# Performance work log

Hardware: AMD Instinct MI355X
Metric: run time of the kernel (lower is better)

The kernel has to match this reference:

```python
import jax, jax.numpy as jnp
import numpy as np

D, H, E, C, B = 1024, 2048, 8, 1024, 8192


def setup_inputs() -> dict:
    key = jax.random.key(0)
    ks = jax.random.split(key, 12)
    s_d = 1.0 / np.sqrt(D)
    s_h = 1.0 / np.sqrt(H)
    return {
        "x": jax.random.normal(ks[0], (B, D), dtype=jnp.float32),
        # gate (Router): Linear(D,D) -> relu -> Linear(D,E) -> softmax
        "gate_w1": jax.random.normal(ks[1], (D, D), dtype=jnp.float32) * s_d,
        "gate_b1": jax.random.normal(ks[2], (D,), dtype=jnp.float32) * s_d,
        "gate_w2": jax.random.normal(ks[3], (D, E), dtype=jnp.float32) * s_d,
        "gate_b2": jax.random.normal(ks[4], (E,), dtype=jnp.float32) * s_d,
        # experts stacked: fc1 [E,D,H], fc2 [E,H,H]
        "W1": jax.random.normal(ks[5], (E, D, H), dtype=jnp.float32) * s_d,
        "b1": jax.random.normal(ks[6], (E, H), dtype=jnp.float32) * s_d,
        "W2": jax.random.normal(ks[7], (E, H, H), dtype=jnp.float32) * s_h,
        "b2": jax.random.normal(ks[8], (E, H), dtype=jnp.float32) * s_h,
        # classifier Linear(H, C)
        "clf_w": jax.random.normal(ks[9], (H, C), dtype=jnp.float32) * s_h,
        "clf_b": jax.random.normal(ks[10], (C,), dtype=jnp.float32) * s_h,
    }


def reference(x, gate_w1, gate_b1, gate_w2, gate_b2, W1, b1, W2, b2, clf_w, clf_b):
    # Router: softmax over experts (dim=1)
    g = jax.nn.relu(x @ gate_w1 + gate_b1)          # [B, D]
    scores = jax.nn.softmax(g @ gate_w2 + gate_b2, axis=1)  # [B, E]

    # All experts, dense (training-mode forward): batched GEMMs over E
    h = jax.nn.relu(jnp.einsum('bd,edh->beh', x, W1) + b1[None])   # [B, E, H]
    expert_outs = jnp.einsum('beh,ehk->bek', h, W2) + b2[None]      # [B, E, H]

    # Shared classifier applied per (token, expert)
    logits = jnp.einsum('beh,hc->bec', expert_outs, clf_w) + clf_b  # [B, E, C]
    return logits, scores
```

## Files before the change

### kernel.cpp

```cpp
#include <hip/hip_runtime.h>
#include <stdint.h>

#define B_DIM 8192
#define D_DIM 1024
#define H_DIM 2048
#define E_DIM 8
#define C_DIM 1024

typedef _Float16 f16x8 __attribute__((ext_vector_type(8)));
typedef float f32x4 __attribute__((ext_vector_type(4)));

__device__ __forceinline__ void store_val(float* p, float v) { *p = v; }
__device__ __forceinline__ void store_val(_Float16* p, float v) { *p = (_Float16)v; }

__device__ __forceinline__ void async_cp16(const void* g, void* l) {
  __builtin_amdgcn_global_load_lds((const __attribute__((address_space(1))) void*)g,
                                   (__attribute__((address_space(3))) void*)l, 16, 0, 0);
}

template <bool RELU, bool BIAS, typename OUT_T>
__global__ void __launch_bounds__(256) gemm_bt(
    const _Float16* __restrict__ A, long aZ,
    const _Float16* __restrict__ Bt, long bZ,
    const float* __restrict__ bias, long biasZ,
    OUT_T* __restrict__ out, long outZ,
    int K, long rs)
{
  __shared__ _Float16 ldsA[128 * 64];
  __shared__ _Float16 ldsB[128 * 64];

  const int z = blockIdx.z;
  A   += (size_t)z * aZ;
  Bt  += (size_t)z * bZ;
  if (BIAS) bias += (size_t)z * biasZ;
  out += (size_t)z * outZ;

  const int tid  = threadIdx.x;
  const int wave = tid >> 6;
  const int lane = tid & 63;
  const int q    = lane >> 4;
  const int l16  = lane & 15;
  const int l8   = lane >> 3;
  const int l7   = lane & 7;

  const int m0   = blockIdx.y * 128;
  const int n0   = blockIdx.x * 128;
  const int wrow = (wave >> 1) * 64;
  const int wcol = (wave & 1) * 64;

  const int swz_st = ((l7 ^ l8) << 3);
  const _Float16* pa[4];
  const _Float16* pb[4];
#pragma unroll
  for (int i = 0; i < 4; ++i) {
    int ci = wave * 4 + i;
    pa[i] = A  + (size_t)(m0 + ci * 8 + l8) * K + swz_st;
    pb[i] = Bt + (size_t)(n0 + ci * 8 + l8) * K + swz_st;
  }

  int a_off[2][4], b_off[2][4];
#pragma unroll
  for (int kk = 0; kk < 2; ++kk) {
#pragma unroll
    for (int r = 0; r < 4; ++r) {
      int sw = ((kk * 4 + q) ^ (l16 & 7)) << 4;
      a_off[kk][r] = (wrow + r * 16 + l16) * 128 + sw;
      b_off[kk][r] = (wcol + r * 16 + l16) * 128 + sw;
    }
  }

  f32x4 acc[4][4];
#pragma unroll
  for (int r = 0; r < 4; ++r)
#pragma unroll
    for (int c = 0; c < 4; ++c)
      acc[r][c] = (f32x4){0.f, 0.f, 0.f, 0.f};

  const char* lAc = (const char*)ldsA;
  const char* lBc = (const char*)ldsB;

  for (int kt = 0; kt < K; kt += 64) {
    __syncthreads();
#pragma unroll
    for (int i = 0; i < 4; ++i) {
      int ci = wave * 4 + i;
      async_cp16(pa[i], ldsA + ci * 512);
      async_cp16(pb[i], ldsB + ci * 512);
      pa[i] += 64;
      pb[i] += 64;
    }
    __syncthreads();
#pragma unroll
    for (int kk = 0; kk < 2; ++kk) {
      f16x8 af[4], bfv[4];
#pragma unroll
      for (int r = 0; r < 4; ++r) af[r]  = *(const f16x8*)(lAc + a_off[kk][r]);
#pragma unroll
      for (int c = 0; c < 4; ++c) bfv[c] = *(const f16x8*)(lBc + b_off[kk][c]);
#pragma unroll
      for (int r = 0; r < 4; ++r)
#pragma unroll
        for (int c = 0; c < 4; ++c)
          acc[r][c] = __builtin_amdgcn_mfma_f32_16x16x32_f16(af[r], bfv[c], acc[r][c], 0, 0, 0);
    }
  }

#pragma unroll
  for (int c = 0; c < 4; ++c) {
    int col = n0 + wcol + c * 16 + l16;
    float bv = BIAS ? bias[col] : 0.f;
#pragma unroll
    for (int r = 0; r < 4; ++r) {
      int row = m0 + wrow + r * 16 + q * 4;
      f32x4 v = acc[r][c];
#pragma unroll
      for (int i = 0; i < 4; ++i) {
        float xv = v[i] + bv;
        if (RELU) xv = fmaxf(xv, 0.f);
        store_val(out + (size_t)(row + i) * rs + col, xv);
      }
    }
  }
}

template <bool RELU, bool BIAS, typename OUT_T, int K_CT>
__global__ void __launch_bounds__(512) gemm256(
    const _Float16* __restrict__ A, long aZ,
    const _Float16* __restrict__ Bt, long bZ,
    const float* __restrict__ bias, long biasZ,
    OUT_T* __restrict__ out, long outZ, long rs)
{
  constexpr int NT = K_CT / 64;
  __shared__ _Float16 ldsA[2 * 256 * 64];
  __shared__ _Float16 ldsB[2 * 256 * 64];

  const int z = blockIdx.z;
  A   += (size_t)z * aZ;
  Bt  += (size_t)z * bZ;
  if (BIAS) bias += (size_t)z * biasZ;
  out += (size_t)z * outZ;

  const int nwg = gridDim.x * gridDim.y;
  const int wg  = blockIdx.y * gridDim.x + blockIdx.x;
  const int sw  = (wg & 7) * (nwg >> 3) + (wg >> 3);
  const int bx  = sw % gridDim.x;
  const int by  = sw / gridDim.x;

  const int tid  = threadIdx.x;
  const int wave = tid >> 6;
  const int lane = tid & 63;
  const int q    = lane >> 4;
  const int l16  = lane & 15;
  const int l8   = lane >> 3;
  const int l7   = lane & 7;

  const int m0   = by * 256;
  const int n0   = bx * 256;
  const int wm   = wave >> 2;
  const int wn   = wave & 3;
  const int wrow = wm * 128;
  const int wcol = wn * 64;

  const int swz_st = ((l7 ^ l8) << 3);
  const _Float16* paB = A  + (size_t)(m0 + wave * 16 + l8) * K_CT + swz_st;
  const _Float16* pbB = Bt + (size_t)(n0 + wave * 16 + l8) * K_CT + swz_st;

  int a_base[2], b_base[2];
#pragma unroll
  for (int kk = 0; kk < 2; ++kk) {
    int swr = (((kk * 4 + q) ^ (l16 & 7)) << 4);
    a_base[kk] = (wrow + l16) * 128 + swr;
    b_base[kk] = (wcol + l16) * 128 + swr;
  }

  f32x4 acc[8][4];
#pragma unroll
  for (int r = 0; r < 8; ++r)
#pragma unroll
    for (int c = 0; c < 4; ++c)
      acc[r][c] = (f32x4){0.f, 0.f, 0.f, 0.f};

  const char* lA = (const char*)ldsA;
  const char* lB = (const char*)ldsB;

#define STAGE_A(bufe, hh, ptr)                                                        \
  {                                                                                   \
    _Pragma("unroll")                                                                 \
    for (int i_ = 0; i_ < 2; ++i_)                                                    \
      async_cp16((ptr) + (size_t)((hh) * 128 + i_ * 8) * K_CT,                        \
                 (void*)(ldsA + (bufe) + (hh) * 8192 + (wave * 2 + i_) * 512));       \
  }
#define STAGE_B(bufe, hh, ptr)                                                        \
  {                                                                                   \
    _Pragma("unroll")                                                                 \
    for (int i_ = 0; i_ < 2; ++i_)                                                    \
      async_cp16((ptr) + (size_t)((hh) * 128 + i_ * 8) * K_CT,                        \
                 (void*)(ldsB + (bufe) + (hh) * 8192 + (wave * 2 + i_) * 512));       \
  }

  STAGE_A(0, 0, paB) STAGE_A(0, 1, paB)
  STAGE_B(0, 0, pbB) STAGE_B(0, 1, pbB)
  asm volatile("s_waitcnt vmcnt(0)" ::: "memory");
  __builtin_amdgcn_s_barrier();

  f16x8 afA[4], afB[4], bfv0[4], bfv1[4];
#pragma unroll
  for (int r = 0; r < 4; ++r) afA[r]  = *(const f16x8*)(lA + a_base[0] + r * 2048);
#pragma unroll
  for (int c = 0; c < 4; ++c) bfv0[c] = *(const f16x8*)(lB + b_base[0] + c * 2048);

  const _Float16* pa_t = paB + 64;
  const _Float16* pb_t = pbB + 64;

  for (int t = 0; t < NT; ++t) {
    const int bofs  = (t & 1) * 32768;
    const int nofs  = bofs ^ 32768;
    const int nbufe = ((t + 1) & 1) * 16384;

#pragma unroll
    for (int r = 0; r < 4; ++r) afB[r]  = *(const f16x8*)(lA + bofs + a_base[1] + r * 2048);
#pragma unroll
    for (int c = 0; c < 4; ++c) bfv1[c] = *(const f16x8*)(lB + bofs + b_base[1] + c * 2048);
    if (t + 1 < NT) { STAGE_A(nbufe, 0, pa_t) STAGE_A(nbufe, 1, pa_t) }
    __builtin_amdgcn_s_setprio(1);
#pragma unroll
    for (int c = 0; c < 4; ++c)
#pragma unroll
      for (int r = 0; r < 4; ++r)
        acc[r][c] = __builtin_amdgcn_mfma_f32_16x16x32_f16(afA[r], bfv0[c], acc[r][c], 0, 0, 0);
    __builtin_amdgcn_s_setprio(0);
    __builtin_amdgcn_s_barrier();

#pragma unroll
    for (int r = 0; r < 4; ++r) afA[r] = *(const f16x8*)(lA + bofs + a_base[0] + (4 + r) * 2048);
    if (t + 1 < NT) { STAGE_B(nbufe, 0, pb_t) STAGE_B(nbufe, 1, pb_t) }
    __builtin_amdgcn_s_setprio(1);
#pragma unroll
    for (int c = 0; c < 4; ++c)
#pragma unroll
      for (int r = 0; r < 4; ++r)
        acc[r][c] = __builtin_amdgcn_mfma_f32_16x16x32_f16(afB[r], bfv1[c], acc[r][c], 0, 0, 0);
    __builtin_amdgcn_s_setprio(0);
    __builtin_amdgcn_s_barrier();

#pragma unroll
    for (int r = 0; r < 4; ++r) afB[r] = *(const f16x8*)(lA + bofs + a_base[1] + (4 + r) * 2048);
    __builtin_amdgcn_s_setprio(1);
#pragma unroll
    for (int c = 0; c < 4; ++c)
#pragma unroll
      for (int r = 0; r < 4; ++r)
        acc[4 + r][c] = __builtin_amdgcn_mfma_f32_16x16x32_f16(afA[r], bfv0[c], acc[4 + r][c], 0, 0, 0);
    __builtin_amdgcn_s_setprio(0);
    asm volatile("s_waitcnt vmcnt(0)" ::: "memory");
    __builtin_amdgcn_s_barrier();

    if (t + 1 < NT) {
#pragma unroll
      for (int r = 0; r < 4; ++r) afA[r]  = *(const f16x8*)(lA + nofs + a_base[0] + r * 2048);
#pragma unroll
      for (int c = 0; c < 4; ++c) bfv0[c] = *(const f16x8*)(lB + nofs + b_base[0] + c * 2048);
    }
    __builtin_amdgcn_s_setprio(1);
#pragma unroll
    for (int c = 0; c < 4; ++c)
#pragma unroll
      for (int r = 0; r < 4; ++r)
        acc[4 + r][c] = __builtin_amdgcn_mfma_f32_16x16x32_f16(afB[r], bfv1[c], acc[4 + r][c], 0, 0, 0);
    __builtin_amdgcn_s_setprio(0);
    __builtin_amdgcn_s_barrier();

    pa_t += 64;
    pb_t += 64;
  }
#undef STAGE_A
#undef STAGE_B

#pragma unroll
  for (int c = 0; c < 4; ++c) {
    int col = n0 + wcol + c * 16 + l16;
    float bv = BIAS ? bias[col] : 0.f;
#pragma unroll
    for (int r = 0; r < 8; ++r) {
      int row = m0 + wrow + r * 16 + q * 4;
      f32x4 v = acc[r][c];
#pragma unroll
      for (int i = 0; i < 4; ++i) {
        float xv = v[i] + bv;
        if (RELU) xv = fmaxf(xv, 0.f);
        store_val(out + (size_t)(row + i) * rs + col, xv);
      }
    }
  }
}

__global__ void cast_f32_f16(const float* __restrict__ in, _Float16* __restrict__ out, int n) {
  int i = (blockIdx.x * blockDim.x + threadIdx.x) * 4;
  if (i >= n) return;
  float4 v = *(const float4*)(in + i);
  union { _Float16 h[4]; uint2 u; } r;
  r.h[0] = (_Float16)v.x; r.h[1] = (_Float16)v.y;
  r.h[2] = (_Float16)v.z; r.h[3] = (_Float16)v.w;
  *(uint2*)(out + i) = r.u;
}

__global__ void transpose_cast(const float* __restrict__ in, _Float16* __restrict__ out,
                               int R, int Cn) {
  __shared__ float tile[32][33];
  in  += (size_t)blockIdx.z * R * Cn;
  out += (size_t)blockIdx.z * R * Cn;
  int c0 = blockIdx.x * 32, r0 = blockIdx.y * 32;
  int tx = threadIdx.x, ty = threadIdx.y;
#pragma unroll
  for (int i = ty; i < 32; i += 8)
    tile[i][tx] = in[(size_t)(r0 + i) * Cn + c0 + tx];
  __syncthreads();
#pragma unroll
  for (int i = ty; i < 32; i += 8)
    out[(size_t)(c0 + i) * R + r0 + tx] = (_Float16)tile[tx][i];
}

__global__ void gate2_softmax(const _Float16* __restrict__ g, const float* __restrict__ w2,
                              const float* __restrict__ b2, float* __restrict__ scores) {
  int wv   = threadIdx.x >> 6;
  int lane = threadIdx.x & 63;
  int b    = blockIdx.x * 4 + wv;
  const _Float16* gr = g + (size_t)b * D_DIM;
  float acc[8];
#pragma unroll
  for (int e = 0; e < 8; ++e) acc[e] = 0.f;
#pragma unroll
  for (int half = 0; half < 2; ++half) {
    int d0 = lane * 8 + half * 512;
    f16x8 gv = *(const f16x8*)(gr + d0);
#pragma unroll
    for (int j = 0; j < 8; ++j) {
      float gx = (float)gv[j];
#pragma unroll
      for (int e = 0; e < 8; ++e) acc[e] += gx * w2[(d0 + j) * 8 + e];
    }
  }
#pragma unroll
  for (int s = 32; s > 0; s >>= 1)
#pragma unroll
    for (int e = 0; e < 8; ++e) acc[e] += __shfl_xor(acc[e], s);
  if (lane == 0) {
    float mx = acc[0] + b2[0];
    float v[8];
    v[0] = mx;
#pragma unroll
    for (int e = 1; e < 8; ++e) { v[e] = acc[e] + b2[e]; mx = fmaxf(mx, v[e]); }
    float ex[8], sum = 0.f;
#pragma unroll
    for (int e = 0; e < 8; ++e) { ex[e] = expf(v[e] - mx); sum += ex[e]; }
    float inv = 1.f / sum;
#pragma unroll
    for (int e = 0; e < 8; ++e) scores[(size_t)b * 8 + e] = ex[e] * inv;
  }
}

__global__ void combined_bias(const float* __restrict__ b2, const float* __restrict__ cw,
                              const float* __restrict__ cb, float* __restrict__ bc) {
  int e  = blockIdx.y;
  int cl = threadIdx.x & 63;
  int c  = blockIdx.x * 64 + cl;
  int ks = threadIdx.x >> 6;
  float acc = 0.f;
  for (int k = ks; k < H_DIM; k += 4)
    acc += b2[e * H_DIM + k] * cw[(size_t)k * C_DIM + c];
  __shared__ float red[256];
  red[threadIdx.x] = acc;
  __syncthreads();
  if (ks == 0)
    bc[(size_t)e * C_DIM + c] = red[cl] + red[cl + 64] + red[cl + 128] + red[cl + 192] + cb[c];
}

extern "C" void kernel_launch(void* const* d_in, const int* in_sizes, int n_in,
                              void* d_out, int out_size, void* d_ws, size_t ws_size,
                              hipStream_t stream) {
  const float* x   = (const float*)d_in[0];
  const float* gw1 = (const float*)d_in[1];
  const float* gb1 = (const float*)d_in[2];
  const float* gw2 = (const float*)d_in[3];
  const float* gb2 = (const float*)d_in[4];
  const float* W1  = (const float*)d_in[5];
  const float* b1  = (const float*)d_in[6];
  const float* W2  = (const float*)d_in[7];
  const float* b2  = (const float*)d_in[8];
  const float* cw  = (const float*)d_in[9];
  const float* cb  = (const float*)d_in[10];

  char* ws = (char*)d_ws;
  _Float16* xb     = (_Float16*)(ws);
  _Float16* g      = (_Float16*)(ws + 16777216ull);
  _Float16* gw1t   = (_Float16*)(ws + 33554432ull);
  _Float16* W1t    = (_Float16*)(ws + 35651584ull);
  _Float16* W2c    = (_Float16*)(ws + 69206016ull);
  _Float16* cwt    = (_Float16*)(ws + 136314880ull);
  _Float16* WcombT = (_Float16*)(ws + 140509184ull);
  float*    bc     = (float*)   (ws + 174063616ull);
  _Float16* h_all  = (_Float16*)(ws + 174096384ull);

  float* logits = (float*)d_out;
  float* scores = logits + (size_t)B_DIM * E_DIM * C_DIM;

  cast_f32_f16<<<B_DIM * D_DIM / 4 / 256, 256, 0, stream>>>(x, xb, B_DIM * D_DIM);
  transpose_cast<<<dim3(32, 32, 1), dim3(32, 8), 0, stream>>>(gw1, gw1t, D_DIM, D_DIM);
  transpose_cast<<<dim3(64, 32, 8), dim3(32, 8), 0, stream>>>(W1, W1t, D_DIM, H_DIM);
  cast_f32_f16<<<E_DIM * H_DIM * H_DIM / 4 / 256, 256, 0, stream>>>(W2, W2c, E_DIM * H_DIM * H_DIM);
  transpose_cast<<<dim3(32, 64, 1), dim3(32, 8), 0, stream>>>(cw, cwt, H_DIM, C_DIM);

  gemm_bt<true, true, _Float16><<<dim3(8, 64, 1), 256, 0, stream>>>(
      xb, 0, gw1t, 0, gb1, 0, g, 0, D_DIM, (long)D_DIM);
  gate2_softmax<<<B_DIM / 4, 256, 0, stream>>>(g, gw2, gb2, scores);

  gemm256<false, false, _Float16, H_DIM><<<dim3(8, 4, 8), 512, 0, stream>>>(
      cwt, 0, W2c, (long)H_DIM * H_DIM, nullptr, 0,
      WcombT, (long)C_DIM * H_DIM, (long)H_DIM);
  combined_bias<<<dim3(C_DIM / 64, E_DIM), 256, 0, stream>>>(b2, cw, cb, bc);

  gemm256<true, true, _Float16, D_DIM><<<dim3(8, 32, 8), 512, 0, stream>>>(
      xb, 0, W1t, (long)H_DIM * D_DIM, b1, (long)H_DIM,
      h_all, (long)B_DIM * H_DIM, (long)H_DIM);

  gemm256<false, true, float, H_DIM><<<dim3(4, 32, 8), 512, 0, stream>>>(
      h_all, (long)B_DIM * H_DIM, WcombT, (long)C_DIM * H_DIM, bc, (long)C_DIM,
      logits, (long)C_DIM, (long)(E_DIM * C_DIM));
}
```

Measured before the change: 1.443 ms.

## Shrink gemm256 K-tile to 32 with new swizzle and move Wcomb GEMM to gemm_bt

The 256x256 GEMM kernel now stages K in chunks of 32 instead of 64, which halves LDS use per buffer, uses a new XOR swizzle, and simplifies the pipeline to two MFMA phases per iteration. The intent is lower LDS footprint, which may allow more resident workgroups and less register pressure. The trade-off is twice as many loop iterations and barriers, and less latency hiding per stage. The small combined-weight GEMM is also moved to the 128-tile gemm_bt kernel to give it a larger grid.

```diff
diff --git a/kernel.cpp b/kernel.cpp
--- a/kernel.cpp
+++ b/kernel.cpp
@@ -130,9 +130,9 @@
     const float* __restrict__ bias, long biasZ,
     OUT_T* __restrict__ out, long outZ, long rs)
 {
-  constexpr int NT = K_CT / 64;
-  __shared__ _Float16 ldsA[2 * 256 * 64];
-  __shared__ _Float16 ldsB[2 * 256 * 64];
+  constexpr int NT = K_CT / 32;
+  __shared__ _Float16 ldsA[2 * 256 * 32];
+  __shared__ _Float16 ldsB[2 * 256 * 32];
 
   const int z = blockIdx.z;
   A   += (size_t)z * aZ;
@@ -151,8 +151,6 @@
   const int lane = tid & 63;
   const int q    = lane >> 4;
   const int l16  = lane & 15;
-  const int l8   = lane >> 3;
-  const int l7   = lane & 7;
 
   const int m0   = by * 256;
   const int n0   = bx * 256;
@@ -161,16 +159,26 @@
   const int wrow = wm * 128;
   const int wcol = wn * 64;
 
-  const int swz_st = ((l7 ^ l8) << 3);
-  const _Float16* paB = A  + (size_t)(m0 + wave * 16 + l8) * K_CT + swz_st;
-  const _Float16* pbB = Bt + (size_t)(n0 + wave * 16 + l8) * K_CT + swz_st;
-
-  int a_base[2], b_base[2];
-#pragma unroll
-  for (int kk = 0; kk < 2; ++kk) {
-    int swr = (((kk * 4 + q) ^ (l16 & 7)) << 4);
-    a_base[kk] = (wrow + l16) * 128 + swr;
-    b_base[kk] = (wcol + l16) * 128 + swr;
+  const int sw8 = (((lane & 3) ^ ((lane >> 3) & 3)) << 3);
+  const _Float16* pa[2];
+  const _Float16* pb[2];
+#pragma unroll
+  for (int i = 0; i < 2; ++i) {
+    int r0 = (wave * 2 + i) * 16;
+    pa[i] = A  + (size_t)(m0 + r0 + (lane >> 2)) * K_CT + sw8;
+    pb[i] = Bt + (size_t)(n0 + r0 + (lane >> 2)) * K_CT + sw8;
+  }
+
+  int a_off[8], b_off[4];
+#pragma unroll
+  for (int r = 0; r < 8; ++r) {
+    int row = wrow + r * 16 + l16;
+    a_off[r] = row * 64 + ((q ^ ((row >> 1) & 3)) << 4);
+  }
+#pragma unroll
+  for (int c = 0; c < 4; ++c) {
+    int row = wcol + c * 16 + l16;
+    b_off[c] = row * 64 + ((q ^ ((row >> 1) & 3)) << 4);
   }
 
   f32x4 acc[8][4];
@@ -183,98 +191,59 @@
   const char* lA = (const char*)ldsA;
   const char* lB = (const char*)ldsB;
 
-#define STAGE_A(bufe, hh, ptr)                                                        \
-  {                                                                                   \
-    _Pragma("unroll")                                                                 \
-    for (int i_ = 0; i_ < 2; ++i_)                                                    \
-      async_cp16((ptr) + (size_t)((hh) * 128 + i_ * 8) * K_CT,                        \
-                 (void*)(ldsA + (bufe) + (hh) * 8192 + (wave * 2 + i_) * 512));       \
-  }
-#define STAGE_B(bufe, hh, ptr)                                                        \
-  {                                                                                   \
-    _Pragma("unroll")                                                                 \
-    for (int i_ = 0; i_ < 2; ++i_)                                                    \
-      async_cp16((ptr) + (size_t)((hh) * 128 + i_ * 8) * K_CT,                        \
-                 (void*)(ldsB + (bufe) + (hh) * 8192 + (wave * 2 + i_) * 512));       \
-  }
-
-  STAGE_A(0, 0, paB) STAGE_A(0, 1, paB)
-  STAGE_B(0, 0, pbB) STAGE_B(0, 1, pbB)
+#pragma unroll
+  for (int i = 0; i < 2; ++i) {
+    int ci = wave * 2 + i;
+    async_cp16(pa[i], ldsA + ci * 512);
+    async_cp16(pb[i], ldsB + ci * 512);
+    pa[i] += 32;
+    pb[i] += 32;
+  }
   asm volatile("s_waitcnt vmcnt(0)" ::: "memory");
   __builtin_amdgcn_s_barrier();
 
-  f16x8 afA[4], afB[4], bfv0[4], bfv1[4];
-#pragma unroll
-  for (int r = 0; r < 4; ++r) afA[r]  = *(const f16x8*)(lA + a_base[0] + r * 2048);
-#pragma unroll
-  for (int c = 0; c < 4; ++c) bfv0[c] = *(const f16x8*)(lB + b_base[0] + c * 2048);
-
-  const _Float16* pa_t = paB + 64;
-  const _Float16* pb_t = pbB + 64;
-
   for (int t = 0; t < NT; ++t) {
-    const int bofs  = (t & 1) * 32768;
-    const int nofs  = bofs ^ 32768;
-    const int nbufe = ((t + 1) & 1) * 16384;
-
-#pragma unroll
-    for (int r = 0; r < 4; ++r) afB[r]  = *(const f16x8*)(lA + bofs + a_base[1] + r * 2048);
-#pragma unroll
-    for (int c = 0; c < 4; ++c) bfv1[c] = *(const f16x8*)(lB + bofs + b_base[1] + c * 2048);
-    if (t + 1 < NT) { STAGE_A(nbufe, 0, pa_t) STAGE_A(nbufe, 1, pa_t) }
+    const int bofs  = (t & 1) * 16384;
+    const int nbufe = ((t + 1) & 1) * 8192;
+
+    f16x8 af[4], bf[4];
+#pragma unroll
+    for (int r = 0; r < 4; ++r) af[r] = *(const f16x8*)(lA + bofs + a_off[r]);
+#pragma unroll
+    for (int c = 0; c < 4; ++c) bf[c] = *(const f16x8*)(lB + bofs + b_off[c]);
+    if (t + 1 < NT) {
+#pragma unroll
+      for (int i = 0; i < 2; ++i) {
+        int ci = wave * 2 + i;
+        async_cp16(pa[i], ldsA + nbufe + ci * 512);
+        async_cp16(pb[i], ldsB + nbufe + ci * 512);
+      }
+    }
     __builtin_amdgcn_s_setprio(1);
 #pragma unroll
     for (int c = 0; c < 4; ++c)
 #pragma unroll
       for (int r = 0; r < 4; ++r)
-        acc[r][c] = __builtin_amdgcn_mfma_f32_16x16x32_f16(afA[r], bfv0[c], acc[r][c], 0, 0, 0);
+        acc[r][c] = __builtin_amdgcn_mfma_f32_16x16x32_f16(af[r], bf[c], acc[r][c], 0, 0, 0);
     __builtin_amdgcn_s_setprio(0);
     __builtin_amdgcn_s_barrier();
 
-#pragma unroll
-    for (int r = 0; r < 4; ++r) afA[r] = *(const f16x8*)(lA + bofs + a_base[0] + (4 + r) * 2048);
-    if (t + 1 < NT) { STAGE_B(nbufe, 0, pb_t) STAGE_B(nbufe, 1, pb_t) }
+    f16x8 af2[4];
+#pragma unroll
+    for (int r = 0; r < 4; ++r) af2[r] = *(const f16x8*)(lA + bofs + a_off[4 + r]);
     __builtin_amdgcn_s_setprio(1);
 #pragma unroll
     for (int c = 0; c < 4; ++c)
 #pragma unroll
       for (int r = 0; r < 4; ++r)
-        acc[r][c] = __builtin_amdgcn_mfma_f32_16x16x32_f16(afB[r], bfv1[c], acc[r][c], 0, 0, 0);
-    __builtin_amdgcn_s_setprio(0);
-    __builtin_amdgcn_s_barrier();
-
-#pragma unroll
-    for (int r = 0; r < 4; ++r) afB[r] = *(const f16x8*)(lA + bofs + a_base[1] + (4 + r) * 2048);
-    __builtin_amdgcn_s_setprio(1);
-#pragma unroll
-    for (int c = 0; c < 4; ++c)
-#pragma unroll
-      for (int r = 0; r < 4; ++r)
-        acc[4 + r][c] = __builtin_amdgcn_mfma_f32_16x16x32_f16(afA[r], bfv0[c], acc[4 + r][c], 0, 0, 0);
+        acc[4 + r][c] = __builtin_amdgcn_mfma_f32_16x16x32_f16(af2[r], bf[c], acc[4 + r][c], 0, 0, 0);
     __builtin_amdgcn_s_setprio(0);
     asm volatile("s_waitcnt vmcnt(0)" ::: "memory");
     __builtin_amdgcn_s_barrier();
 
-    if (t + 1 < NT) {
-#pragma unroll
-      for (int r = 0; r < 4; ++r) afA[r]  = *(const f16x8*)(lA + nofs + a_base[0] + r * 2048);
-#pragma unroll
-      for (int c = 0; c < 4; ++c) bfv0[c] = *(const f16x8*)(lB + nofs + b_base[0] + c * 2048);
-    }
-    __builtin_amdgcn_s_setprio(1);
-#pragma unroll
-    for (int c = 0; c < 4; ++c)
-#pragma unroll
-      for (int r = 0; r < 4; ++r)
-        acc[4 + r][c] = __builtin_amdgcn_mfma_f32_16x16x32_f16(afB[r], bfv1[c], acc[4 + r][c], 0, 0, 0);
-    __builtin_amdgcn_s_setprio(0);
-    __builtin_amdgcn_s_barrier();
-
-    pa_t += 64;
-    pb_t += 64;
-  }
-#undef STAGE_A
-#undef STAGE_B
+#pragma unroll
+    for (int i = 0; i < 2; ++i) { pa[i] += 32; pb[i] += 32; }
+  }
 
 #pragma unroll
   for (int c = 0; c < 4; ++c) {
@@ -414,9 +383,9 @@
       xb, 0, gw1t, 0, gb1, 0, g, 0, D_DIM, (long)D_DIM);
   gate2_softmax<<<B_DIM / 4, 256, 0, stream>>>(g, gw2, gb2, scores);
 
-  gemm256<false, false, _Float16, H_DIM><<<dim3(8, 4, 8), 512, 0, stream>>>(
+  gemm_bt<false, false, _Float16><<<dim3(16, 8, 8), 256, 0, stream>>>(
       cwt, 0, W2c, (long)H_DIM * H_DIM, nullptr, 0,
-      WcombT, (long)C_DIM * H_DIM, (long)H_DIM);
+      WcombT, (long)C_DIM * H_DIM, H_DIM, (long)H_DIM);
   combined_bias<<<dim3(C_DIM / 64, E_DIM), 256, 0, stream>>>(b2, cw, cb, bc);
 
   gemm256<true, true, _Float16, D_DIM><<<dim3(8, 32, 8), 512, 0, stream>>>(
```

Measured after the change: 1.427 ms. About the same (-1.1%).
